# Kernel tuning notes

Hardware: AMD Instinct MI355X
Metric: run time of the kernel (lower is better)

Reference implementation:

```python
import jax, jax.numpy as jnp
import numpy as np
import math

QUERY_DIM = 512
FEAT_DIM = 2048
HID_DIM = 512
OUT_DIM = 512
B, L, S, T = 32, 128, 36, 36


def _linear_params(key, d_in, d_out):
    kw, kb = jax.random.split(key)
    scale = 1.0 / math.sqrt(d_in)
    W = jax.random.uniform(kw, (d_in, d_out), jnp.float32, -scale, scale)
    b = jax.random.uniform(kb, (d_out,), jnp.float32, -scale, scale)
    return W, b


def setup_inputs() -> dict:
    key = jax.random.key(0)
    ks = jax.random.split(key, 9)
    query = jax.random.normal(ks[0], (B, L, QUERY_DIM), jnp.float32)
    src = jax.random.normal(ks[1], (B, S, FEAT_DIM), jnp.float32)
    trg = jax.random.normal(ks[2], (B, T, FEAT_DIM), jnp.float32)
    Wq, bq = _linear_params(ks[3], QUERY_DIM, HID_DIM)
    Ws, bs = _linear_params(ks[4], FEAT_DIM, HID_DIM)
    Wt, bt = _linear_params(ks[5], FEAT_DIM, HID_DIM)
    Wsv, bsv = _linear_params(ks[6], FEAT_DIM, HID_DIM)
    Wtv, btv = _linear_params(ks[7], FEAT_DIM, HID_DIM)
    Wo, bo = _linear_params(ks[8], HID_DIM * 2 + QUERY_DIM, OUT_DIM)
    return dict(query=query, src=src, trg=trg,
                Wq=Wq, bq=bq, Ws=Ws, bs=bs, Wt=Wt, bt=bt,
                Wsv=Wsv, bsv=bsv, Wtv=Wtv, btv=btv, Wo=Wo, bo=bo)


def reference(query, src, trg, Wq, bq, Ws, bs, Wt, bt, Wsv, bsv, Wtv, btv, Wo, bo):
    b, l, _ = query.shape
    s = src.shape[1]
    t = trg.shape[1]
    q = query @ Wq + bq                      # (b, l, h)
    s_key = src @ Ws + bs                    # (b, s, h)
    t_key = trg @ Wt + bt                    # (b, t, h)
    # Faithful to torch: s_key.unsqueeze(1) + t_key.unsqueeze(2) -> (b, t, s, h),
    # then labeled 'istk' in the einsum (requires s == t).
    rel_key = (s_key[:, None, :, :] + t_key[:, :, None, :]) * 0.5  # (b, t, s, h)
    weight = jnp.einsum('blk,bstk->blst', q, rel_key) / math.sqrt(HID_DIM)
    weight = jax.nn.softmax(weight.reshape(b, l, s * t), axis=-1).reshape(b, l, s, t)
    s_value = src @ Wsv + bsv                # (b, s, h)
    t_value = trg @ Wtv + btv                # (b, t, h)
    s_ctx = jnp.einsum('blst,bsh->blh', weight, s_value)
    t_ctx = jnp.einsum('blst,bth->blh', weight, t_value)
    x = jnp.concatenate((query, s_ctx, t_ctx), axis=-1)
    return jax.nn.relu(x @ Wo + bo)
```

## Files before the change

### kernel.cpp

```cpp
#include <hip/hip_runtime.h>
#include <hip/hip_bf16.h>
#include <math.h>

#define DEVI __device__ __forceinline__

typedef __attribute__((ext_vector_type(4))) float f32x4;
typedef __attribute__((ext_vector_type(8))) short bf16x8;

DEVI unsigned short f2bf(float f) {
  union { float f; unsigned int u; } v; v.f = f;
  return (unsigned short)((v.u + 0x7FFFu + ((v.u >> 16) & 1u)) >> 16);
}
DEVI float bf2f(unsigned short s) {
  union { unsigned int u; float f; } v; v.u = ((unsigned int)s) << 16; return v.f;
}
DEVI bf16x8 pack8(f32x4 a, f32x4 b) {
  bf16x8 r;
  r[0] = (short)f2bf(a[0]); r[1] = (short)f2bf(a[1]);
  r[2] = (short)f2bf(a[2]); r[3] = (short)f2bf(a[3]);
  r[4] = (short)f2bf(b[0]); r[5] = (short)f2bf(b[1]);
  r[6] = (short)f2bf(b[2]); r[7] = (short)f2bf(b[3]);
  return r;
}
DEVI void gload16(const unsigned short* g, unsigned short* l) {
  __builtin_amdgcn_global_load_lds(
      (const __attribute__((address_space(1))) unsigned int*)g,
      (__attribute__((address_space(3))) unsigned int*)l, 16, 0, 0);
}
#define SBAR() do { asm volatile("" ::: "memory"); \
                    __builtin_amdgcn_s_barrier();  \
                    asm volatile("" ::: "memory"); } while (0)

struct PrepJobs {
  const float* src[9];
  unsigned short* dst[9];
  int K[9];
  int base[9];
  int type[9];
};

__global__ __launch_bounds__(256) void prep(PrepJobs J) {
  __shared__ float t[64][65];
  int tile = blockIdx.x;
  int job = 0;
  while (job < 8 && tile >= J.base[job + 1]) ++job;
  int tl = tile - J.base[job];
  int K = J.K[job];
  if (J.type[job] == 0) {
    int tn = tl & 7, tk = tl >> 3;
    int x = threadIdx.x & 63, y = threadIdx.x >> 6;
    const float* s = J.src[job];
    int k0 = tk * 64, n0 = tn * 64;
#pragma unroll
    for (int yy = y; yy < 64; yy += 4)
      t[yy][x] = s[(size_t)(k0 + yy) * 512 + n0 + x];
    __syncthreads();
    unsigned short* d = J.dst[job];
    int kb = (x >> 3) & 7, ko = x & 7;
#pragma unroll
    for (int yy = y; yy < 64; yy += 4) {
      int n = n0 + yy;
      int kswz = k0 + (((kb + n) & 7) << 3) + ko;
      d[(size_t)n * K + kswz] = f2bf(t[x][yy]);
    }
  } else {
    int nk = K >> 6;
    int rt = tl / nk;
    int r0 = rt * 64, k0 = (tl - rt * nk) * 64;
    int r = threadIdx.x >> 2, kq = threadIdx.x & 3;
    int row = r0 + r;
    const float* s = J.src[job] + (size_t)row * K + k0 + kq * 16;
    f32x4 a0 = *(const f32x4*)s;
    f32x4 a1 = *(const f32x4*)(s + 4);
    f32x4 a2 = *(const f32x4*)(s + 8);
    f32x4 a3 = *(const f32x4*)(s + 12);
    unsigned short* d = J.dst[job] + (size_t)row * K + k0;
    int kb0 = kq * 2;
    *(bf16x8*)(d + ((kb0 + row) & 7) * 8) = pack8(a0, a1);
    *(bf16x8*)(d + ((kb0 + 1 + row) & 7) * 8) = pack8(a2, a3);
  }
}

struct GJob {
  const unsigned short* A0;
  const unsigned short* Bt;
  const float* bias;
  unsigned short* Cb;
  int Astride, Bstride, Cstride, nTilesN, nt, mode, tileBase;
};
struct GBatch { GJob j[7]; int njobs; int swz; };

template <int MI, int NI>
__global__ __launch_bounds__(256) void gemm_pipe(GBatch batch) {
  constexpr int BM = MI * 32, BN = NI * 32;
  int gt = blockIdx.x;
  if (batch.swz) {
    int cpx = gridDim.x >> 3;
    gt = (blockIdx.x & 7) * cpx + (blockIdx.x >> 3);
  }
  int job = 0;
#pragma unroll
  for (int i = 1; i < 7; ++i)
    if (i < batch.njobs && gt >= batch.j[i].tileBase) job = i;
  GJob J = batch.j[job];
  int tl = gt - J.tileBase;
  int bm = (tl / J.nTilesN) * BM, bn = (tl % J.nTilesN) * BN;

  __shared__ __align__(16) unsigned short La[2][BM * 64];
  __shared__ __align__(16) unsigned short Lb[2][BN * 64];

  int tid = threadIdx.x;
  int wave = tid >> 6, lane = tid & 63;
  int lrow = lane & 15, lq = lane >> 4;
  int wr = (wave >> 1) * (MI * 16), wc = (wave & 1) * (NI * 16);
  f32x4 acc[MI][NI] = {};

  int nt = J.nt;

  auto stage_both = [&](int t, int buf) {
    const unsigned short* GA = J.A0 + (size_t)bm * J.Astride + (size_t)(t << 6);
    const unsigned short* GB = J.Bt + (size_t)bn * J.Bstride + (size_t)(t << 6);
#pragma unroll
    for (int p = 0; p < MI; ++p) {
      int s = p * 256 + tid;
      gload16(GA + (size_t)(s >> 3) * J.Astride + (s & 7) * 8,
              &La[buf][(size_t)(p * 256 + wave * 64) * 8]);
    }
#pragma unroll
    for (int p = 0; p < NI; ++p) {
      int s = p * 256 + tid;
      gload16(GB + (size_t)(s >> 3) * J.Bstride + (s & 7) * 8,
              &Lb[buf][(size_t)(p * 256 + wave * 64) * 8]);
    }
  };

  stage_both(0, 0);
  if (nt > 1) stage_both(1, 1);

  for (int t = 0; t < nt; ++t) {
    if (t + 1 < nt) {
      if constexpr (MI + NI == 8)      asm volatile("s_waitcnt vmcnt(8)" ::: "memory");
      else if constexpr (MI + NI == 6) asm volatile("s_waitcnt vmcnt(6)" ::: "memory");
      else                             asm volatile("s_waitcnt vmcnt(4)" ::: "memory");
    } else {
      asm volatile("s_waitcnt vmcnt(0)" ::: "memory");
    }
    SBAR();
    int cur = t & 1;
    __builtin_amdgcn_s_setprio(1);
#pragma unroll
    for (int kc = 0; kc < 2; ++kc) {
      int kb = kc * 4 + lq;
      bf16x8 af[MI], bv[NI];
#pragma unroll
      for (int mi = 0; mi < MI; ++mi) {
        int r = wr + mi * 16 + lrow;
        af[mi] = *(const bf16x8*)&La[cur][r * 64 + ((kb + r) & 7) * 8];
      }
#pragma unroll
      for (int ni = 0; ni < NI; ++ni) {
        int r = wc + ni * 16 + lrow;
        bv[ni] = *(const bf16x8*)&Lb[cur][r * 64 + ((kb + r) & 7) * 8];
      }
#pragma unroll
      for (int mi = 0; mi < MI; ++mi)
#pragma unroll
        for (int ni = 0; ni < NI; ++ni)
          acc[mi][ni] = __builtin_amdgcn_mfma_f32_16x16x32_bf16(af[mi], bv[ni], acc[mi][ni], 0, 0, 0);
    }
    __builtin_amdgcn_s_setprio(0);
    SBAR();
    if (t + 2 < nt) stage_both(t + 2, cur);
  }

#pragma unroll
  for (int mi = 0; mi < MI; ++mi) {
#pragma unroll
    for (int ni = 0; ni < NI; ++ni) {
      int gn = bn + wc + ni * 16 + lrow;
      float bvs = J.bias ? J.bias[gn] : 0.f;
      int gm0 = bm + wr + mi * 16 + lq * 4;
      if (J.mode == 0) {
#pragma unroll
        for (int r = 0; r < 4; ++r)
          J.Cb[(size_t)(gm0 + r) * J.Cstride + gn] = f2bf(acc[mi][ni][r] + bvs);
      } else {
#pragma unroll
        for (int r = 0; r < 4; ++r) {
          int row = gm0 + r;
          int col = (gn & ~63) | (((((gn >> 3) & 7) + row) & 7) << 3) | (gn & 7);
          J.Cb[(size_t)row * J.Cstride + col] = f2bf(acc[mi][ni][r] + bvs);
        }
      }
    }
  }
}

struct HJob {
  const unsigned short* A0;
  const unsigned short* Bt;
  unsigned short* Cb;
  int Astride, Bstride, Cstride, nTilesN, nt, tileBase;
};
struct S3Args {
  HJob g[2];
  int nGemm;
  const unsigned short* qh;
  const unsigned short* s_key;
  const unsigned short* t_key;
  float* Wsw;
  float* Wtw;
};

__global__ __launch_bounds__(256) void stage3(S3Args A) {
  __shared__ __align__(16) unsigned short SH[2][8192];
  int tid = threadIdx.x;
  int wave = tid >> 6, lane = tid & 63;
  int lrow = lane & 15, lq = lane >> 4;

  if ((int)blockIdx.x < A.nGemm) {
    int gt = blockIdx.x;
    HJob J = (gt >= A.g[1].tileBase) ? A.g[1] : A.g[0];
    int tl = gt - J.tileBase;
    int bm = (tl / J.nTilesN) * 64, bn = (tl % J.nTilesN) * 64;
    int wr = (wave >> 1) * 32, wc = (wave & 1) * 32;
    f32x4 acc[2][2] = {};
    int nt = J.nt;

    auto stage2 = [&](int t, int buf) {
      const unsigned short* GA = J.A0 + (size_t)bm * J.Astride + (size_t)(t << 6);
      const unsigned short* GB = J.Bt + (size_t)bn * J.Bstride + (size_t)(t << 6);
#pragma unroll
      for (int p = 0; p < 2; ++p) {
        int s = p * 256 + tid;
        gload16(GA + (size_t)(s >> 3) * J.Astride + (s & 7) * 8,
                &SH[buf][(size_t)(p * 256 + wave * 64) * 8]);
      }
#pragma unroll
      for (int p = 0; p < 2; ++p) {
        int s = p * 256 + tid;
        gload16(GB + (size_t)(s >> 3) * J.Bstride + (s & 7) * 8,
                &SH[buf][4096 + (size_t)(p * 256 + wave * 64) * 8]);
      }
    };

    stage2(0, 0);
    if (nt > 1) stage2(1, 1);

    for (int t = 0; t < nt; ++t) {
      if (t + 1 < nt) asm volatile("s_waitcnt vmcnt(4)" ::: "memory");
      else            asm volatile("s_waitcnt vmcnt(0)" ::: "memory");
      SBAR();
      int cur = t & 1;
      __builtin_amdgcn_s_setprio(1);
#pragma unroll
      for (int kc = 0; kc < 2; ++kc) {
        int kb = kc * 4 + lq;
        bf16x8 af[2], bv[2];
#pragma unroll
        for (int mi = 0; mi < 2; ++mi) {
          int r = wr + mi * 16 + lrow;
          af[mi] = *(const bf16x8*)&SH[cur][r * 64 + ((kb + r) & 7) * 8];
        }
#pragma unroll
        for (int ni = 0; ni < 2; ++ni) {
          int r = wc + ni * 16 + lrow;
          bv[ni] = *(const bf16x8*)&SH[cur][4096 + r * 64 + ((kb + r) & 7) * 8];
        }
#pragma unroll
        for (int mi = 0; mi < 2; ++mi)
#pragma unroll
          for (int ni = 0; ni < 2; ++ni)
            acc[mi][ni] = __builtin_amdgcn_mfma_f32_16x16x32_bf16(af[mi], bv[ni], acc[mi][ni], 0, 0, 0);
      }
      __builtin_amdgcn_s_setprio(0);
      SBAR();
      if (t + 2 < nt) stage2(t + 2, cur);
    }
#pragma unroll
    for (int mi = 0; mi < 2; ++mi) {
#pragma unroll
      for (int ni = 0; ni < 2; ++ni) {
        int gn = bn + wc + ni * 16 + lrow;
        int gm0 = bm + wr + mi * 16 + lq * 4;
#pragma unroll
        for (int r = 0; r < 4; ++r)
          J.Cb[(size_t)(gm0 + r) * J.Cstride + gn] = f2bf(acc[mi][ni][r]);
      }
    }
  } else {
    float (*red)[3][64][4] = (float(*)[3][64][4])&SH[0][0];
    int bid2 = blockIdx.x - A.nGemm;
    int b = bid2 >> 3, lc = bid2 & 7;
    int mat = wave >> 1, kh = wave & 1;
    int row0 = b * 128 + lc * 16;
    const unsigned short* qp = A.qh + (size_t)row0 * 512;
    const unsigned short* key = (mat ? A.s_key : A.t_key) + (size_t)b * 36 * 512;
    f32x4 acc[3] = {};
    for (int kc = kh * 8; kc < kh * 8 + 8; ++kc) {
      int k = kc * 32 + lq * 8;
      bf16x8 af = *(const bf16x8*)(qp + (size_t)lrow * 512 + k);
#pragma unroll
      for (int nf = 0; nf < 3; ++nf) {
        int n = nf * 16 + lrow; if (n > 35) n = 35;
        bf16x8 bv = *(const bf16x8*)(key + (size_t)n * 512 + k);
        acc[nf] = __builtin_amdgcn_mfma_f32_16x16x32_bf16(af, bv, acc[nf], 0, 0, 0);
      }
    }
#pragma unroll
    for (int nf = 0; nf < 3; ++nf)
      *(f32x4*)&red[wave][nf][lane][0] = acc[nf];
    __syncthreads();

    if (kh == 0) {
      const float ccs = 0.022097086912079608f;
      float ex[3][4];
#pragma unroll
      for (int r = 0; r < 4; ++r) {
        float a0 = (red[wave][0][lane][r] + red[wave + 1][0][lane][r]) * ccs;
        float a1 = (red[wave][1][lane][r] + red[wave + 1][1][lane][r]) * ccs;
        float a2 = (lrow < 4)
            ? (red[wave][2][lane][r] + red[wave + 1][2][lane][r]) * ccs : -1e30f;
        float mx = fmaxf(fmaxf(a0, a1), a2);
        for (int s = 1; s < 16; s <<= 1) mx = fmaxf(mx, __shfl_xor(mx, s));
        float e0 = __expf(a0 - mx), e1 = __expf(a1 - mx);
        float e2 = (lrow < 4) ? __expf(a2 - mx) : 0.f;
        float sum = e0 + e1 + e2;
        for (int s = 1; s < 16; s <<= 1) sum += __shfl_xor(sum, s);
        float inv = 1.f / sum;
        ex[0][r] = e0 * inv; ex[1][r] = e1 * inv; ex[2][r] = e2 * inv;
      }
      float* W = mat ? A.Wtw : A.Wsw;
#pragma unroll
      for (int nf = 0; nf < 3; ++nf) {
        int col = nf * 16 + lrow;
        if (col < 36) {
#pragma unroll
          for (int r = 0; r < 4; ++r)
            W[(size_t)(row0 + lq * 4 + r) * 36 + col] = ex[nf][r];
        }
      }
    }
  }
}

__global__ __launch_bounds__(256) void wsum(
    const float* __restrict__ Wsw, const float* __restrict__ Wtw,
    const unsigned short* __restrict__ svp, const unsigned short* __restrict__ tvp,
    const unsigned short* __restrict__ Pb, float* __restrict__ out) {
  __shared__ float wlT[2][36][16];
  int b = blockIdx.x, lc = blockIdx.y;
  int h0 = blockIdx.z << 8;
  int tid = threadIdx.x;
  int row0 = b * 128 + lc * 16;
  for (int i = tid; i < 2 * 16 * 36; i += 256) {
    int m = i / 576, rem = i - m * 576;
    int l = rem / 36, j = rem - l * 36;
    wlT[m][j][l] = (m ? Wtw : Wsw)[(size_t)(row0 + l) * 36 + j];
  }
  __syncthreads();

  int lgrp = tid >> 5;
  int hgrp = tid & 31;
  float a2[2][8] = {};
#pragma unroll
  for (int m = 0; m < 2; ++m) {
    const unsigned short* V = (m ? tvp : svp) + (size_t)b * 36 * 512 + h0;
    for (int j = 0; j < 36; ++j) {
      float w0 = wlT[m][j][lgrp * 2];
      float w1 = wlT[m][j][lgrp * 2 + 1];
      bf16x8 v = *(const bf16x8*)(V + (size_t)j * 512 + hgrp * 8);
      float vf[8];
#pragma unroll
      for (int hi = 0; hi < 8; ++hi) vf[hi] = bf2f((unsigned short)v[hi]);
#pragma unroll
      for (int hi = 0; hi < 8; ++hi) {
        a2[0][hi] += w0 * vf[hi];
        a2[1][hi] += w1 * vf[hi];
      }
    }
  }
#pragma unroll
  for (int li = 0; li < 2; ++li) {
    int R = row0 + lgrp * 2 + li;
    bf16x8 p = *(const bf16x8*)(Pb + (size_t)R * 512 + h0 + hgrp * 8);
    float* op = out + (size_t)R * 512 + h0 + hgrp * 8;
    f32x4 o0, o1;
#pragma unroll
    for (int hi = 0; hi < 4; ++hi) {
      o0[hi] = fmaxf(bf2f((unsigned short)p[hi]) + a2[li][hi], 0.f);
      o1[hi] = fmaxf(bf2f((unsigned short)p[4 + hi]) + a2[li][4 + hi], 0.f);
    }
    *(f32x4*)op = o0;
    *(f32x4*)(op + 4) = o1;
  }
}

extern "C" void kernel_launch(void* const* d_in, const int* in_sizes, int n_in,
                              void* d_out, int out_size, void* d_ws, size_t ws_size,
                              hipStream_t stream) {
  (void)in_sizes; (void)n_in; (void)out_size; (void)ws_size;
  const float* query = (const float*)d_in[0];
  const float* src   = (const float*)d_in[1];
  const float* trg   = (const float*)d_in[2];
  const float* Wq  = (const float*)d_in[3];  const float* bq  = (const float*)d_in[4];
  const float* Wsk = (const float*)d_in[5];  const float* bs  = (const float*)d_in[6];
  const float* Wtk = (const float*)d_in[7];  const float* bt  = (const float*)d_in[8];
  const float* Wsv = (const float*)d_in[9];  const float* bsv = (const float*)d_in[10];
  const float* Wtv = (const float*)d_in[11]; const float* btv = (const float*)d_in[12];
  const float* Wo  = (const float*)d_in[13]; const float* bo  = (const float*)d_in[14];

  unsigned short* WqT    = (unsigned short*)d_ws;
  unsigned short* WsT    = WqT  + 512 * 512;
  unsigned short* WtT    = WsT  + 512 * 2048;
  unsigned short* WsvT   = WtT  + 512 * 2048;
  unsigned short* WtvT   = WsvT + 512 * 2048;
  unsigned short* WoT    = WtvT + 512 * 2048;
  unsigned short* queryB = WoT  + 512 * 1536;
  unsigned short* srcB   = queryB + 4096 * 512;
  unsigned short* trgB   = srcB + 1152 * 2048;
  unsigned short* qh     = trgB + 1152 * 2048;
  unsigned short* s_key  = qh + 4096 * 512;
  unsigned short* t_key  = s_key + 1152 * 512;
  unsigned short* s_val  = t_key + 1152 * 512;
  unsigned short* t_val  = s_val + 1152 * 512;
  unsigned short* svp    = t_val + 1152 * 512;
  unsigned short* tvp    = svp + 1152 * 512;
  unsigned short* Pb     = tvp + 1152 * 512;
  float* Wsw = (float*)(Pb + 4096 * 512);
  float* Wtw = Wsw + 4096 * 36;
  float* out = (float*)d_out;

  PrepJobs pj;
  const float* psrc[9] = { Wq, Wsk, Wtk, Wsv, Wtv, Wo, query, src, trg };
  unsigned short* pdst[9] = { WqT, WsT, WtT, WsvT, WtvT, WoT, queryB, srcB, trgB };
  int pK[9]    = { 512, 2048, 2048, 2048, 2048, 1536, 512, 2048, 2048 };
  int ptype[9] = { 0, 0, 0, 0, 0, 0, 1, 1, 1 };
  int prows[9] = { 0, 0, 0, 0, 0, 0, 4096, 1152, 1152 };
  int pbase = 0;
  for (int i = 0; i < 9; ++i) {
    pj.src[i] = psrc[i]; pj.dst[i] = pdst[i]; pj.K[i] = pK[i]; pj.type[i] = ptype[i];
    pj.base[i] = pbase;
    pbase += ptype[i] ? (prows[i] / 64) * (pK[i] / 64) : (pK[i] / 64) * 8;
  }
  prep<<<pbase, 256, 0, stream>>>(pj);

  {
    GBatch pb;
    pb.swz = 0;
    int base = 0;
    const unsigned short* Aarr[4] = { srcB, trgB, srcB, trgB };
    const unsigned short* Barr[4] = { WsT, WtT, WsvT, WtvT };
    const float* biasArr[4] = { bs, bt, bsv, btv };
    unsigned short* Carr[4] = { s_key, t_key, s_val, t_val };
    for (int i = 0; i < 4; ++i) {
      GJob& j = pb.j[i];
      j.A0 = Aarr[i]; j.Bt = Barr[i]; j.bias = biasArr[i]; j.Cb = Carr[i];
      j.Astride = 2048; j.Bstride = 2048; j.Cstride = 512;
      j.nTilesN = 4; j.nt = 32; j.mode = (i < 2) ? 0 : 2;
      j.tileBase = base; base += 18 * 4;
    }
    {
      GJob& j = pb.j[4];
      j.A0 = queryB; j.Bt = WqT; j.bias = bq; j.Cb = qh;
      j.Astride = 512; j.Bstride = 512; j.Cstride = 512;
      j.nTilesN = 4; j.nt = 8; j.mode = 0;
      j.tileBase = base; base += 64 * 4;
    }
    {
      GJob& j = pb.j[5];
      j.A0 = queryB; j.Bt = WoT; j.bias = bo; j.Cb = Pb;
      j.Astride = 512; j.Bstride = 1536; j.Cstride = 512;
      j.nTilesN = 4; j.nt = 8; j.mode = 0;
      j.tileBase = base; base += 64 * 4;
    }
    pb.j[6] = pb.j[5]; pb.j[6].tileBase = 0x7fffffff;
    pb.njobs = 6;
    gemm_pipe<2, 4><<<base, 256, 0, stream>>>(pb);
  }

  {
    S3Args sa;
    HJob& a = sa.g[0];
    a.A0 = s_val; a.Bt = WoT + 512; a.Cb = svp;
    a.Astride = 512; a.Bstride = 1536; a.Cstride = 512;
    a.nTilesN = 8; a.nt = 8; a.tileBase = 0;
    HJob& b2 = sa.g[1];
    b2 = a;
    b2.A0 = t_val; b2.Bt = WoT + 1024; b2.Cb = tvp;
    b2.tileBase = 18 * 8;
    sa.nGemm = 288;
    sa.qh = qh; sa.s_key = s_key; sa.t_key = t_key;
    sa.Wsw = Wsw; sa.Wtw = Wtw;
    stage3<<<288 + 256, 256, 0, stream>>>(sa);
  }

  wsum<<<dim3(32, 8, 2), 256, 0, stream>>>(Wsw, Wtw, svp, tvp, Pb, out);
}
```

Measured before the change: 73.23 us.

## Load GEMM A operand directly into registers, stage only B via LDS

Replaces the templated LDS double-buffered GEMM with a specialized 64x128 kernel where each lane loads its A fragments straight from global memory into registers (pre-swizzled layout), and only B goes through LDS via async global-to-LDS loads. The main loop is unrolled by two with separate register buffers, and launch bounds request 4 waves per SIMD for occupancy. This halves LDS footprint and removes A's LDS round trip and its ds_read traffic, at the cost of more VGPRs and less coalesced direct A loads. Loop assumes nt is even.

```diff
diff --git a/kernel.cpp b/kernel.cpp
--- a/kernel.cpp
+++ b/kernel.cpp
@@ -81,102 +81,105 @@
   }
 }
 
-struct GJob {
+struct PJob {
   const unsigned short* A0;
   const unsigned short* Bt;
   const float* bias;
   unsigned short* Cb;
   int Astride, Bstride, Cstride, nTilesN, nt, mode, tileBase;
 };
-struct GBatch { GJob j[7]; int njobs; int swz; };
-
-template <int MI, int NI>
-__global__ __launch_bounds__(256) void gemm_pipe(GBatch batch) {
-  constexpr int BM = MI * 32, BN = NI * 32;
+struct PBatch { PJob j[7]; int njobs; };
+
+__global__ __launch_bounds__(256, 4) void gemm_areg(PBatch batch) {
   int gt = blockIdx.x;
-  if (batch.swz) {
-    int cpx = gridDim.x >> 3;
-    gt = (blockIdx.x & 7) * cpx + (blockIdx.x >> 3);
-  }
   int job = 0;
 #pragma unroll
   for (int i = 1; i < 7; ++i)
     if (i < batch.njobs && gt >= batch.j[i].tileBase) job = i;
-  GJob J = batch.j[job];
+  PJob J = batch.j[job];
   int tl = gt - J.tileBase;
-  int bm = (tl / J.nTilesN) * BM, bn = (tl % J.nTilesN) * BN;
-
-  __shared__ __align__(16) unsigned short La[2][BM * 64];
-  __shared__ __align__(16) unsigned short Lb[2][BN * 64];
+  int bm = (tl / J.nTilesN) * 64, bn = (tl % J.nTilesN) * 128;
+
+  __shared__ __align__(16) unsigned short Lb[2][128 * 64];
 
   int tid = threadIdx.x;
   int wave = tid >> 6, lane = tid & 63;
   int lrow = lane & 15, lq = lane >> 4;
-  int wr = (wave >> 1) * (MI * 16), wc = (wave & 1) * (NI * 16);
-  f32x4 acc[MI][NI] = {};
+  int wr = (wave >> 1) * 32, wc = (wave & 1) * 64;
+  f32x4 acc[2][4] = {};
 
   int nt = J.nt;
 
-  auto stage_both = [&](int t, int buf) {
-    const unsigned short* GA = J.A0 + (size_t)bm * J.Astride + (size_t)(t << 6);
+  const unsigned short* aptr[2][2];
+#pragma unroll
+  for (int mi = 0; mi < 2; ++mi) {
+    int rowg = bm + wr + mi * 16 + lrow;
+#pragma unroll
+    for (int kc = 0; kc < 2; ++kc) {
+      int kb = kc * 4 + lq;
+      aptr[mi][kc] = J.A0 + (size_t)rowg * J.Astride + ((kb + rowg) & 7) * 8;
+    }
+  }
+
+  bf16x8 RA0[2][2], RA1[2][2];
+
+  auto aload = [&](int t, bf16x8 (&RA)[2][2]) {
+#pragma unroll
+    for (int mi = 0; mi < 2; ++mi)
+#pragma unroll
+      for (int kc = 0; kc < 2; ++kc)
+        RA[mi][kc] = *(const bf16x8*)(aptr[mi][kc] + (t << 6));
+  };
+  auto bdma = [&](int t, int buf) {
     const unsigned short* GB = J.Bt + (size_t)bn * J.Bstride + (size_t)(t << 6);
 #pragma unroll
-    for (int p = 0; p < MI; ++p) {
-      int s = p * 256 + tid;
-      gload16(GA + (size_t)(s >> 3) * J.Astride + (s & 7) * 8,
-              &La[buf][(size_t)(p * 256 + wave * 64) * 8]);
-    }
-#pragma unroll
-    for (int p = 0; p < NI; ++p) {
+    for (int p = 0; p < 4; ++p) {
       int s = p * 256 + tid;
       gload16(GB + (size_t)(s >> 3) * J.Bstride + (s & 7) * 8,
               &Lb[buf][(size_t)(p * 256 + wave * 64) * 8]);
     }
   };
-
-  stage_both(0, 0);
-  if (nt > 1) stage_both(1, 1);
-
-  for (int t = 0; t < nt; ++t) {
-    if (t + 1 < nt) {
-      if constexpr (MI + NI == 8)      asm volatile("s_waitcnt vmcnt(8)" ::: "memory");
-      else if constexpr (MI + NI == 6) asm volatile("s_waitcnt vmcnt(6)" ::: "memory");
-      else                             asm volatile("s_waitcnt vmcnt(4)" ::: "memory");
-    } else {
-      asm volatile("s_waitcnt vmcnt(0)" ::: "memory");
-    }
-    SBAR();
-    int cur = t & 1;
+  auto compute = [&](int buf, const bf16x8 (&RA)[2][2]) {
     __builtin_amdgcn_s_setprio(1);
 #pragma unroll
     for (int kc = 0; kc < 2; ++kc) {
       int kb = kc * 4 + lq;
-      bf16x8 af[MI], bv[NI];
-#pragma unroll
-      for (int mi = 0; mi < MI; ++mi) {
-        int r = wr + mi * 16 + lrow;
-        af[mi] = *(const bf16x8*)&La[cur][r * 64 + ((kb + r) & 7) * 8];
-      }
-#pragma unroll
-      for (int ni = 0; ni < NI; ++ni) {
+      bf16x8 bv[4];
+#pragma unroll
+      for (int ni = 0; ni < 4; ++ni) {
         int r = wc + ni * 16 + lrow;
-        bv[ni] = *(const bf16x8*)&Lb[cur][r * 64 + ((kb + r) & 7) * 8];
-      }
-#pragma unroll
-      for (int mi = 0; mi < MI; ++mi)
-#pragma unroll
-        for (int ni = 0; ni < NI; ++ni)
-          acc[mi][ni] = __builtin_amdgcn_mfma_f32_16x16x32_bf16(af[mi], bv[ni], acc[mi][ni], 0, 0, 0);
+        bv[ni] = *(const bf16x8*)&Lb[buf][r * 64 + ((kb + r) & 7) * 8];
+      }
+#pragma unroll
+      for (int mi = 0; mi < 2; ++mi)
+#pragma unroll
+        for (int ni = 0; ni < 4; ++ni)
+          acc[mi][ni] = __builtin_amdgcn_mfma_f32_16x16x32_bf16(RA[mi][kc], bv[ni], acc[mi][ni], 0, 0, 0);
     }
     __builtin_amdgcn_s_setprio(0);
+  };
+
+  aload(0, RA0); bdma(0, 0);
+  aload(1, RA1); bdma(1, 1);
+
+  for (int t = 0; t < nt; t += 2) {
+    asm volatile("s_waitcnt vmcnt(8)" ::: "memory");
     SBAR();
-    if (t + 2 < nt) stage_both(t + 2, cur);
-  }
-
-#pragma unroll
-  for (int mi = 0; mi < MI; ++mi) {
-#pragma unroll
-    for (int ni = 0; ni < NI; ++ni) {
+    compute(0, RA0);
+    SBAR();
+    if (t + 2 < nt) { aload(t + 2, RA0); bdma(t + 2, 0); }
+    if (t + 2 < nt) asm volatile("s_waitcnt vmcnt(8)" ::: "memory");
+    else            asm volatile("s_waitcnt vmcnt(0)" ::: "memory");
+    SBAR();
+    compute(1, RA1);
+    SBAR();
+    if (t + 3 < nt) { aload(t + 3, RA1); bdma(t + 3, 1); }
+  }
+
+#pragma unroll
+  for (int mi = 0; mi < 2; ++mi) {
+#pragma unroll
+    for (int ni = 0; ni < 4; ++ni) {
       int gn = bn + wc + ni * 16 + lrow;
       float bvs = J.bias ? J.bias[gn] : 0.f;
       int gm0 = bm + wr + mi * 16 + lq * 4;
@@ -446,29 +449,28 @@
   prep<<<pbase, 256, 0, stream>>>(pj);
 
   {
-    GBatch pb;
-    pb.swz = 0;
+    PBatch pb;
     int base = 0;
     const unsigned short* Aarr[4] = { srcB, trgB, srcB, trgB };
     const unsigned short* Barr[4] = { WsT, WtT, WsvT, WtvT };
     const float* biasArr[4] = { bs, bt, bsv, btv };
     unsigned short* Carr[4] = { s_key, t_key, s_val, t_val };
     for (int i = 0; i < 4; ++i) {
-      GJob& j = pb.j[i];
+      PJob& j = pb.j[i];
       j.A0 = Aarr[i]; j.Bt = Barr[i]; j.bias = biasArr[i]; j.Cb = Carr[i];
       j.Astride = 2048; j.Bstride = 2048; j.Cstride = 512;
       j.nTilesN = 4; j.nt = 32; j.mode = (i < 2) ? 0 : 2;
       j.tileBase = base; base += 18 * 4;
     }
     {
-      GJob& j = pb.j[4];
+      PJob& j = pb.j[4];
       j.A0 = queryB; j.Bt = WqT; j.bias = bq; j.Cb = qh;
       j.Astride = 512; j.Bstride = 512; j.Cstride = 512;
       j.nTilesN = 4; j.nt = 8; j.mode = 0;
       j.tileBase = base; base += 64 * 4;
     }
     {
-      GJob& j = pb.j[5];
+      PJob& j = pb.j[5];
       j.A0 = queryB; j.Bt = WoT; j.bias = bo; j.Cb = Pb;
       j.Astride = 512; j.Bstride = 1536; j.Cstride = 512;
       j.nTilesN = 4; j.nt = 8; j.mode = 0;
@@ -476,7 +478,7 @@
     }
     pb.j[6] = pb.j[5]; pb.j[6].tileBase = 0x7fffffff;
     pb.njobs = 6;
-    gemm_pipe<2, 4><<<base, 256, 0, stream>>>(pb);
+    gemm_areg<<<base, 256, 0, stream>>>(pb);
   }
 
   {
```

New measurement: 78.79 us. +7.6%, slower.
